# Kernel tuning notes

Measured on AMD Instinct MI355X. Metric: run time of the kernel, lower is better.

Reference implementation:

```python
import jax, jax.numpy as jnp
import numpy as np

L = 3          # atom_decoder_depth
HEADS = 8      # spatial attention heads
T_HEADS = 8    # temporal attention heads
WQ = 32        # atoms_per_window_queries
HK = 128       # atoms_per_window_keys
EPS = 1e-5


def _ln(x, g=None, b=None):
    mu = jnp.mean(x, -1, keepdims=True)
    v = jnp.mean((x - mu) ** 2, -1, keepdims=True)
    xn = (x - mu) * jax.lax.rsqrt(v + EPS)
    if g is not None:
        xn = xn * g + b
    return xn


def _adaln(a, s, w_sc, b_sc, w_sk):
    # adaptive LN: sigmoid-scaled normed activations + conditioned skip
    sn = _ln(s)
    return jax.nn.sigmoid(sn @ w_sc + b_sc) * _ln(a) + sn @ w_sk


def setup_inputs() -> dict:
    key = jax.random.key(0)
    ks = iter(jax.random.split(key, 64))
    B0, T, N, M, D, TS = 1, 8, 1024, 4096, 256, 768
    HID = 2 * D

    def rn(shape, s=1.0):
        return jax.random.normal(next(ks), shape, jnp.float32) * s

    NW = (M + WQ - 1) // WQ
    a = rn((B0 * T, N, 2 * TS))
    q = rn((B0 * T, M, D))
    c = rn((B0 * T, M, D))
    atom_dec_bias = rn((B0, NW, WQ, HK, L * HEADS), 0.1)
    tok_idx = jnp.sort(jax.random.randint(next(ks), (B0, M), 0, N), axis=-1)
    atom_to_token = jax.nn.one_hot(tok_idx, N, dtype=jnp.float32)
    atom_pad_mask = jnp.ones((B0, M), bool)
    timestamps = jnp.sort(jax.random.uniform(next(ks), (B0, T)) * 10.0, axis=-1)
    p = 0.02
    return dict(
        a=a, q=q, c=c, atom_dec_bias=atom_dec_bias,
        atom_to_token=atom_to_token, atom_pad_mask=atom_pad_mask,
        timestamps=timestamps,
        W_a2q=rn((2 * TS, D), p),
        ada1_sw=rn((L, D, D), p), ada1_sb=rn((L, D), p), ada1_kw=rn((L, D, D), p),
        attn_wq=rn((L, D, D), p), attn_bq=rn((L, D), p),
        attn_wk=rn((L, D, D), p), attn_wv=rn((L, D, D), p),
        attn_wg=rn((L, D, D), p), attn_wo=rn((L, D, D), p),
        og_w=rn((L, D, D), p), og_b=rn((L, D), p),
        ada2_sw=rn((L, D, D), p), ada2_sb=rn((L, D), p), ada2_kw=rn((L, D, D), p),
        tr_w1=rn((L, D, HID), p), tr_w2=rn((L, D, HID), p), tr_w3=rn((L, HID, D), p),
        tr_gw=rn((L, D, D), p), tr_gb=rn((L, D), p),
        t_ln_g=jnp.ones((L, D)), t_ln_b=jnp.zeros((L, D)),
        t_wq=rn((L, D, D), p), t_wk=rn((L, D, D), p), t_wv=rn((L, D, D), p),
        t_wg=rn((L, D, D), p), t_wo=rn((L, D, D), p),
        t_decay=rn((L, T_HEADS)),
        pos_g=jnp.ones((D,)), pos_b=jnp.zeros((D,)), pos_w=rn((D, 3), p),
        T=8,
    )


def _forward(a, q, c, atom_dec_bias, atom_to_token, atom_pad_mask, timestamps,
             W_a2q, ada1_sw, ada1_sb, ada1_kw, attn_wq, attn_bq, attn_wk,
             attn_wv, attn_wg, attn_wo, og_w, og_b, ada2_sw, ada2_sb, ada2_kw,
             tr_w1, tr_w2, tr_w3, tr_gw, tr_gb, t_ln_g, t_ln_b, t_wq, t_wk,
             t_wv, t_wg, t_wo, t_decay, pos_g, pos_b, pos_w, T):
    BT, N, _ = a.shape
    B0 = BT // T
    M0, D = q.shape[1], q.shape[2]
    NW = (M0 + WQ - 1) // WQ
    M = NW * WQ
    h, dh = HEADS, D // HEADS
    th, tdh = T_HEADS, D // T_HEADS

    # token -> atom gather via one-hot matmul (atom_to_token shared across T)
    a2q = jnp.einsum('bmn,btnd->btmd', atom_to_token,
                     (a @ W_a2q).reshape(B0, T, N, D)).reshape(BT, M0, D)
    q = q + a2q

    pad = M - M0
    qf = jnp.pad(q, ((0, 0), (0, pad), (0, 0)))
    cf = jnp.pad(c, ((0, 0), (0, pad), (0, 0)))
    mask = jnp.pad(atom_pad_mask, ((0, 0), (0, pad)))  # (B0, M)

    side = (HK - WQ) // 2
    # index map: query window w attends keys [w*WQ - side, w*WQ - side + HK)
    widx = jnp.arange(NW)[:, None] * WQ + jnp.arange(HK)[None, :]

    def window_keys(x):  # (B, M, D) -> (B, NW, HK, D)
        xp = jnp.pad(x, ((0, 0), (side, side), (0, 0)))
        return xp[:, widx]

    kmask = jnp.pad(mask, ((0, 0), (side, side)))[:, widx]  # (B0, NW, HK)
    neg = jnp.where(kmask[:, None, :, None, None, :], 0.0, -1e9)

    bias = atom_dec_bias.reshape(B0, NW, WQ, HK, L, HEADS)
    inv_s = 1.0 / np.sqrt(dh).astype(np.float32)
    inv_t = 1.0 / np.sqrt(tdh).astype(np.float32)
    dt = jnp.abs(timestamps[:, :, None] - timestamps[:, None, :])  # (B0,T,T)

    for i in range(L):
        # ---- spatial windowed attention with pair bias ----
        b = _adaln(qf, cf, ada1_sw[i], ada1_sb[i], ada1_kw[i])
        qh = (b @ attn_wq[i] + attn_bq[i]).reshape(BT, NW, WQ, h, dh)
        kin = window_keys(b)                                   # (BT,NW,HK,D)
        kh = (kin @ attn_wk[i]).reshape(BT, NW, HK, h, dh)
        vh = (kin @ attn_wv[i]).reshape(BT, NW, HK, h, dh)
        logits = jnp.einsum('bnqhd,bnkhd->bnhqk', qh, kh) * inv_s
        logits = logits.reshape(B0, T, NW, h, WQ, HK)
        logits = logits + bias[:, :, :, :, i].transpose(0, 1, 4, 2, 3)[:, None] + neg
        p_attn = jax.nn.softmax(logits, axis=-1).reshape(BT, NW, h, WQ, HK)
        o = jnp.einsum('bnhqk,bnkhd->bnqhd', p_attn, vh)
        g = jax.nn.sigmoid(b @ attn_wg[i]).reshape(BT, NW, WQ, h, dh)
        o = (g * o).reshape(BT, M, D) @ attn_wo[i]
        qf = qf + jax.nn.sigmoid(cf @ og_w[i] + og_b[i]) * o
        # conditioned SwiGLU transition
        t = _adaln(qf, cf, ada2_sw[i], ada2_sb[i], ada2_kw[i])
        x = jax.nn.silu(t @ tr_w1[i]) * (t @ tr_w2[i])
        qf = qf + jax.nn.sigmoid(cf @ tr_gw[i] + tr_gb[i]) * (x @ tr_w3[i])
        # ---- temporal attention with per-head decay bias ----
        xt = qf.reshape(B0, T, M, D).transpose(0, 2, 1, 3)     # (B0,M,T,D)
        xn = _ln(xt, t_ln_g[i], t_ln_b[i])
        tq = (xn @ t_wq[i]).reshape(B0, M, T, th, tdh)
        tk = (xn @ t_wk[i]).reshape(B0, M, T, th, tdh)
        tv = (xn @ t_wv[i]).reshape(B0, M, T, th, tdh)
        tl = jnp.einsum('bmqhd,bmkhd->bmhqk', tq, tk) * inv_t
        decay = jax.nn.softplus(t_decay[i])                    # (th,)
        tl = tl - decay[None, None, :, None, None] * dt[:, None, None]
        tp = jax.nn.softmax(tl, axis=-1)
        to = jnp.einsum('bmhqk,bmkhd->bmqhd', tp, tv).reshape(B0, M, T, D)
        tg = jax.nn.sigmoid(xn @ t_wg[i])
        xt = xt + (tg * to) @ t_wo[i]
        qf = xt.transpose(0, 2, 1, 3).reshape(BT, M, D)

    q_out = qf[:, :M0]
    return _ln(q_out, pos_g, pos_b) @ pos_w  # (B*T, M0, 3)


def reference(a, q, c, atom_dec_bias, atom_to_token, atom_pad_mask, timestamps,
              W_a2q, ada1_sw, ada1_sb, ada1_kw, attn_wq, attn_bq, attn_wk,
              attn_wv, attn_wg, attn_wo, og_w, og_b, ada2_sw, ada2_sb, ada2_kw,
              tr_w1, tr_w2, tr_w3, tr_gw, tr_gb, t_ln_g, t_ln_b, t_wq, t_wk,
              t_wv, t_wg, t_wo, t_decay, pos_g, pos_b, pos_w, T):
    return _forward(a, q, c, atom_dec_bias, atom_to_token, atom_pad_mask,
                    timestamps, W_a2q, ada1_sw, ada1_sb, ada1_kw, attn_wq,
                    attn_bq, attn_wk, attn_wv, attn_wg, attn_wo, og_w, og_b,
                    ada2_sw, ada2_sb, ada2_kw, tr_w1, tr_w2, tr_w3, tr_gw,
                    tr_gb, t_ln_g, t_ln_b, t_wq, t_wk, t_wv, t_wg, t_wo,
                    t_decay, pos_g, pos_b, pos_w, T)
```

## Files before the change

### kernel.cpp

```cpp
#include <hip/hip_runtime.h>
#include <cstddef>
#include <cstdint>

#define DEVI __device__ __forceinline__

typedef __attribute__((ext_vector_type(8))) __bf16 bf16x8;
typedef __attribute__((ext_vector_type(8))) unsigned short us8;
typedef __attribute__((ext_vector_type(4))) unsigned short us4;
typedef __attribute__((ext_vector_type(4))) float f32x4;

constexpr int B0_ = 1, T_ = 8, N_ = 1024, M_ = 4096, D_ = 256;
constexpr int BT_ = 8, NW_ = 128, WQ_ = 32, HK_ = 128, SIDE_ = 48;
constexpr int R_ = BT_ * M_;
constexpr size_t Fq = 8388608;

DEVI unsigned short f2b(float f) {
  return __builtin_bit_cast(unsigned short, static_cast<__bf16>(f));
}
DEVI float b2f(unsigned short s) { return __uint_as_float(((unsigned)s) << 16); }
DEVI float sigm(float x) { return 1.0f / (1.0f + __expf(-x)); }
DEVI bf16x8 ld_bf8(const unsigned short* p) {
  return __builtin_bit_cast(bf16x8, *(const us8*)p);
}
DEVI bf16x8 pack_f8(float4 v0, float4 v1) {
  bf16x8 r;
  r[0] = (__bf16)v0.x; r[1] = (__bf16)v0.y; r[2] = (__bf16)v0.z; r[3] = (__bf16)v0.w;
  r[4] = (__bf16)v1.x; r[5] = (__bf16)v1.y; r[6] = (__bf16)v1.z; r[7] = (__bf16)v1.w;
  return r;
}
DEVI void mfma_bf16(f32x4& c, bf16x8 a, bf16x8 b) {
  c = __builtin_amdgcn_mfma_f32_16x16x32_bf16(a, b, c, 0, 0, 0);
}
DEVI void gload16(const void* g, void* l) {
  __builtin_amdgcn_global_load_lds((__attribute__((address_space(1))) void*)g,
                                   (__attribute__((address_space(3))) void*)l, 16, 0, 0);
}

struct ConvArgs {
  const float* src[64];
  int doff[64];
  int Kd[64];
  int Nd[64];
  int n;
};

__global__ __launch_bounds__(256) void conv_k(ConvArgs ca, unsigned short* __restrict__ wbf) {
  int e = blockIdx.x;
  int K = ca.Kd[e], N = ca.Nd[e];
  int nx = N >> 6, nk = K >> 6;
  int t = blockIdx.y;
  if (t >= nx * nk) return;
  int tx = t % nx, tk = t / nx;
  const float* s = ca.src[e];
  unsigned short* d = wbf + ca.doff[e];
  int n = tx * 64 + (threadIdx.x & 63);
  int k0 = tk * 64 + (threadIdx.x >> 6) * 16;
  for (int r = 0; r < 16; r++) {
    int k = k0 + r;
    d[(size_t)n * K + k] = f2b(s[(size_t)k * N + n]);
  }
}

__global__ __launch_bounds__(256) void cvt_k(const float* __restrict__ s,
                                             unsigned short* __restrict__ d, int n8) {
  int i = blockIdx.x * 256 + threadIdx.x;
  if (i >= n8) return;
  float4 v0 = *(const float4*)(s + (size_t)i * 8);
  float4 v1 = *(const float4*)(s + (size_t)i * 8 + 4);
  *(us8*)(d + (size_t)i * 8) = __builtin_bit_cast(us8, pack_f8(v0, v1));
}

__global__ __launch_bounds__(256) void bias_prep_k(
    const float* __restrict__ bq, const float* __restrict__ sb1,
    const float* __restrict__ sb2, const float* __restrict__ ogb,
    const float* __restrict__ trb, float* __restrict__ bias) {
  int t = threadIdx.x;
  for (int i = t; i < 1024 + 3 * 2560; i += 256) bias[i] = 0.f;
  __syncthreads();
  for (int i = 0; i < 3; i++) {
    float* B = bias + 1024 + i * 2560;
    B[t]        = bq[i * 256 + t];
    B[1024 + t] = sb1[i * 256 + t];
    B[1536 + t] = sb2[i * 256 + t];
    B[2048 + t] = ogb[i * 256 + t];
    B[2304 + t] = trb[i * 256 + t];
  }
}

__global__ __launch_bounds__(256) void biasb_k(const float* __restrict__ adb,
                                               unsigned short* __restrict__ biasb) {
  __shared__ float ld[3072];
  int rq = blockIdx.x;
  int t = threadIdx.x;
  const float* src = adb + (size_t)rq * 3072;
  for (int i = t; i < 3072; i += 256) ld[i] = src[i];
  __syncthreads();
  int k = t & 127;
  int pk = (k & 15) * 8 + (k >> 4);
  for (int lh = t >> 7; lh < 24; lh += 2)
    biasb[((size_t)lh * 4096 + rq) * 128 + pk] = f2b(ld[k * 24 + lh]);
}

__global__ __launch_bounds__(256) void tokidx_k(const float* __restrict__ a2t,
                                                int* __restrict__ idx) {
  int m = blockIdx.x * 4 + (threadIdx.x >> 6);
  int lane = threadIdx.x & 63;
  int best = -1;
  for (int j = 0; j < 16; j++) {
    int col = lane * 16 + j;
    if (a2t[(size_t)m * 1024 + col] > 0.5f) best = col;
  }
#pragma unroll
  for (int off = 1; off < 64; off <<= 1) best = max(best, __shfl_xor(best, off));
  if (lane == 0) idx[m] = best;
}

__global__ __launch_bounds__(256) void qfinitln_k(const float* __restrict__ q,
                                                  const unsigned short* __restrict__ tokf,
                                                  const int* __restrict__ idx,
                                                  float* __restrict__ qf,
                                                  unsigned short* __restrict__ lnout) {
  int wid = threadIdx.x >> 6, lane = threadIdx.x & 63;
  size_t row = (size_t)blockIdx.x * 4 + wid;
  int m = (int)(row & 4095);
  int bt = (int)(row >> 12);
  float4 qv = *(const float4*)(q + row * 256 + lane * 4);
  us4 tv = *(const us4*)(tokf + ((size_t)bt * 1024 + idx[m]) * 256 + lane * 4);
  float x[4];
  x[0] = qv.x + b2f(tv[0]); x[1] = qv.y + b2f(tv[1]);
  x[2] = qv.z + b2f(tv[2]); x[3] = qv.w + b2f(tv[3]);
  *(float4*)(qf + row * 256 + lane * 4) = make_float4(x[0], x[1], x[2], x[3]);
  float s = x[0] + x[1] + x[2] + x[3];
  float sq = x[0] * x[0] + x[1] * x[1] + x[2] * x[2] + x[3] * x[3];
#pragma unroll
  for (int o = 1; o < 64; o <<= 1) {
    s += __shfl_xor(s, o);
    sq += __shfl_xor(sq, o);
  }
  float mu = s * 0.00390625f;
  float rs = rsqrtf(sq * 0.00390625f - mu * mu + 1e-5f);
  us4 r;
#pragma unroll
  for (int j = 0; j < 4; j++) r[j] = f2b((x[j] - mu) * rs);
  *(us4*)(lnout + row * 256 + lane * 4) = r;
}

__global__ __launch_bounds__(256) void ln_k(const float* __restrict__ src,
                                            unsigned short* __restrict__ dst) {
  size_t row = (size_t)blockIdx.x * 4 + (threadIdx.x >> 6);
  int lane = threadIdx.x & 63;
  float4 v = ((const float4*)(src + row * 256))[lane];
  float s = v.x + v.y + v.z + v.w;
#pragma unroll
  for (int o = 1; o < 64; o <<= 1) s += __shfl_xor(s, o);
  float mu = s * 0.00390625f;
  float dx = v.x - mu, dy = v.y - mu, dz = v.z - mu, dw = v.w - mu;
  float qv = dx * dx + dy * dy + dz * dz + dw * dw;
#pragma unroll
  for (int o = 1; o < 64; o <<= 1) qv += __shfl_xor(qv, o);
  float rs = rsqrtf(qv * 0.00390625f + 1e-5f);
  us4 r;
  r[0] = f2b(dx * rs); r[1] = f2b(dy * rs); r[2] = f2b(dz * rs); r[3] = f2b(dw * rs);
  *(us4*)(dst + row * 256 + lane * 4) = r;
}

template <int K, int EP, int PAIR>
__global__ __launch_bounds__(256) void gemm4_k(
    const unsigned short* __restrict__ A, const unsigned short* __restrict__ Wt,
    const float* __restrict__ bias, unsigned short* __restrict__ out,
    const unsigned short* __restrict__ lnq, unsigned short* __restrict__ vtb,
    int NOUT) {
  constexpr int NT = K / 64;
  __shared__ __align__(16) unsigned short S[2][16384];
  const int tid = threadIdx.x;
  const int lane = tid & 63, w = tid >> 6;
  const int lg = lane >> 4, lr = lane & 15;
  const int wr = w >> 1, wc = w & 1;
  const size_t m_base = (size_t)blockIdx.x * 128;
  const size_t n_base = (size_t)blockIdx.y * 64;
  const int srow = w * 8 + (lane >> 3);
  const int scol = ((lane & 7) ^ (lane >> 3)) * 8;
  const unsigned short* gA = A + (m_base + srow) * K + scol;
  const unsigned short* gB = Wt + (n_base + srow) * K + scol;
  const unsigned short* gB2 = Wt + (n_base + PAIR + srow) * K + scol;
  f32x4 acc[4][2] = {};
  f32x4 acc2[4][2] = {};
  const int swz = lr & 7;

  auto stage = [&](int buf, int t) {
    unsigned short* Sb = S[buf];
    const int kk = t * 64;
#pragma unroll
    for (int j = 0; j < 4; j++)
      gload16(gA + (size_t)(j * 32) * K + kk, Sb + w * 512 + j * 2048);
#pragma unroll
    for (int j = 0; j < 2; j++)
      gload16(gB + (size_t)(j * 32) * K + kk, Sb + 8192 + w * 512 + j * 2048);
#pragma unroll
    for (int j = 0; j < 2; j++)
      gload16(gB2 + (size_t)(j * 32) * K + kk, Sb + 12288 + w * 512 + j * 2048);
  };
  auto compute = [&](int buf) {
    const unsigned short* Sb = S[buf];
#pragma unroll
    for (int ks = 0; ks < 2; ks++) {
      const int co = ((ks * 4 + lg) ^ swz) << 3;
      bf16x8 af[4], b1[2], b2[2];
#pragma unroll
      for (int i = 0; i < 4; i++)
        af[i] = ld_bf8(Sb + (wr * 64 + i * 16 + lr) * 64 + co);
#pragma unroll
      for (int i = 0; i < 2; i++) {
        b1[i] = ld_bf8(Sb + 8192 + (wc * 32 + i * 16 + lr) * 64 + co);
        b2[i] = ld_bf8(Sb + 12288 + (wc * 32 + i * 16 + lr) * 64 + co);
      }
#pragma unroll
      for (int mi = 0; mi < 4; mi++)
#pragma unroll
        for (int ni = 0; ni < 2; ni++) {
          mfma_bf16(acc[mi][ni], af[mi], b1[ni]);
          mfma_bf16(acc2[mi][ni], af[mi], b2[ni]);
        }
    }
  };

  stage(0, 0);
  __syncthreads();
  int cur = 0;
  for (int t = 0; t < NT - 1; t++) {
    stage(cur ^ 1, t + 1);
    compute(cur);
    __syncthreads();
    cur ^= 1;
  }
  compute(cur);
  __syncthreads();

  unsigned short* St = S[0];
  auto emit_half = [&](int cbase, bool second) {
#pragma unroll
    for (int mi = 0; mi < 4; mi++)
#pragma unroll
      for (int ni = 0; ni < 2; ni++)
#pragma unroll
        for (int r = 0; r < 4; r++) {
          int rowl = wr * 64 + mi * 16 + lg * 4 + r;
          int cl = wc * 32 + ni * 16 + lr;
          float v = (second ? acc2[mi][ni][r] : acc[mi][ni][r]) + bias[cbase + cl];
          St[rowl * 64 + (((cl >> 3) ^ (rowl & 7)) << 3) + (cl & 7)] = f2b(v);
        }
    __syncthreads();
#pragma unroll
    for (int p = 0; p < 4; p++) {
      int rowl = p * 32 + (tid >> 3);
      int chunk = tid & 7;
      us8 v = *(const us8*)(St + rowl * 64 + ((chunk ^ (rowl & 7)) << 3));
      *(us8*)(out + (m_base + rowl) * NOUT + cbase + chunk * 8) = v;
    }
    __syncthreads();
  };

  if constexpr (EP == 1) {
    emit_half((int)n_base, false);
    emit_half((int)n_base + PAIR, true);
  } else if constexpr (EP == 6) {
    emit_half((int)n_base, false);
    if ((int)n_base < 256) {
      const int bt = (int)(m_base >> 12);
      const int m0 = (int)(m_base & 4095);
#pragma unroll
      for (int mi = 0; mi < 4; mi++)
#pragma unroll
        for (int ni = 0; ni < 2; ni++) {
          int cl = wc * 32 + ni * 16 + lr;
          int rowb = wr * 64 + mi * 16 + lg * 4;
          us4 val;
#pragma unroll
          for (int r = 0; r < 4; r++)
            val[r] = f2b(acc2[mi][ni][r] + bias[(int)n_base + cl + 512]);
          *(us4*)(St + cl * 128 + (((rowb >> 3) ^ (cl & 7)) << 3) + (rowb & 7)) = val;
        }
      __syncthreads();
#pragma unroll
      for (int p = 0; p < 4; p++) {
        int cl = tid >> 2;
        int rc = (tid & 3) + p * 4;
        us8 v = *(const us8*)(St + cl * 128 + ((rc ^ (cl & 7)) << 3));
        *(us8*)(vtb + ((size_t)bt * 256 + n_base + cl) * 4096 + m0 + rc * 8) = v;
      }
    } else {
      emit_half((int)n_base + 512, true);
    }
  } else {
#pragma unroll
    for (int mi = 0; mi < 4; mi++)
#pragma unroll
      for (int ni = 0; ni < 2; ni++)
#pragma unroll
        for (int r = 0; r < 4; r++) {
          int rowl = wr * 64 + mi * 16 + lg * 4 + r;
          int cl = wc * 32 + ni * 16 + lr;
          size_t grow = m_base + rowl;
          int gcol = (int)n_base + cl;
          float v = acc[mi][ni][r] + bias[gcol];
          float v2 = acc2[mi][ni][r] + bias[gcol + PAIR];
          unsigned short res;
          if constexpr (EP == 4) {
            res = f2b(sigm(v) * b2f(lnq[grow * 256 + gcol]) + v2);
          } else {
            res = f2b(v * sigm(v) * v2);
          }
          St[rowl * 64 + (((cl >> 3) ^ (rowl & 7)) << 3) + (cl & 7)] = res;
        }
    __syncthreads();
#pragma unroll
    for (int p = 0; p < 4; p++) {
      int rowl = p * 32 + (tid >> 3);
      int chunk = tid & 7;
      us8 v = *(const us8*)(St + rowl * 64 + ((chunk ^ (rowl & 7)) << 3));
      *(us8*)(out + (m_base + rowl) * NOUT + n_base + chunk * 8) = v;
    }
  }
}

template <int K, bool GATED>
__global__ __launch_bounds__(512) void gemmln_k(
    const unsigned short* __restrict__ A, const unsigned short* __restrict__ Wt,
    float* __restrict__ qf, const unsigned short* __restrict__ gate, int goff,
    unsigned short* __restrict__ lnout, const float* __restrict__ lng,
    const float* __restrict__ lnb) {
  constexpr int NT = K / 64;
  __shared__ __align__(16) unsigned short S[2][20480];
  const int tid = threadIdx.x;
  const int lane = tid & 63, w = tid >> 6;
  const int lg = lane >> 4, lr = lane & 15;
  const size_t m_base = (size_t)blockIdx.x * 64;
  const int srow = lane >> 3;
  const int scol = ((lane & 7) ^ srow) * 8;
  const unsigned short* gA = A + (m_base + w * 8 + srow) * K + scol;
  const unsigned short* gB = Wt + (w * 32 + srow) * K + scol;
  f32x4 acc[4][2] = {};
  const int swz = lr & 7;

  auto stage = [&](int buf, int t) {
    unsigned short* Sb = S[buf];
    const int kk = t * 64;
    gload16(gA + kk, Sb + w * 512);
#pragma unroll
    for (int j = 0; j < 4; j++)
      gload16(gB + (size_t)(j * 8) * K + kk, Sb + 4096 + w * 2048 + j * 512);
  };
  auto compute = [&](int buf) {
    const unsigned short* Sb = S[buf];
#pragma unroll
    for (int ks = 0; ks < 2; ks++) {
      const int co = ((ks * 4 + lg) ^ swz) << 3;
      bf16x8 af[4], bf1[2];
#pragma unroll
      for (int i = 0; i < 4; i++) af[i] = ld_bf8(Sb + (i * 16 + lr) * 64 + co);
#pragma unroll
      for (int i = 0; i < 2; i++)
        bf1[i] = ld_bf8(Sb + 4096 + (w * 32 + i * 16 + lr) * 64 + co);
#pragma unroll
      for (int mi = 0; mi < 4; mi++)
#pragma unroll
        for (int ni = 0; ni < 2; ni++) mfma_bf16(acc[mi][ni], af[mi], bf1[ni]);
    }
  };

  stage(0, 0);
  __syncthreads();
  int cur = 0;
  for (int t = 0; t < NT - 1; t++) {
    stage(cur ^ 1, t + 1);
    compute(cur);
    __syncthreads();
    cur ^= 1;
  }
  compute(cur);
  __syncthreads();

  unsigned short* St = S[0];
#pragma unroll
  for (int mi = 0; mi < 4; mi++)
#pragma unroll
    for (int ni = 0; ni < 2; ni++)
#pragma unroll
      for (int r = 0; r < 4; r++) {
        int rowl = mi * 16 + lg * 4 + r;
        int col = w * 32 + ni * 16 + lr;
        size_t grow = m_base + rowl;
        float v = acc[mi][ni][r];
        if constexpr (GATED) v *= sigm(b2f(gate[grow * 512 + goff + col]));
        float nq = qf[grow * 256 + col] + v;
        qf[grow * 256 + col] = nq;
        St[rowl * 256 + (((col >> 3) ^ (rowl & 7)) << 3) + (col & 7)] = f2b(nq);
      }
  __syncthreads();
  float gv[4], bv[4];
  if (lng) {
#pragma unroll
    for (int j = 0; j < 4; j++) {
      gv[j] = lng[lane * 4 + j];
      bv[j] = lnb[lane * 4 + j];
    }
  }
  const int rchunk = lane >> 1;
  const int rsub = (lane & 1) << 2;
  for (int rr = 0; rr < 8; rr++) {
    int rowl = w * 8 + rr;
    us4 vv = *(const us4*)(St + rowl * 256 + ((rchunk ^ (rowl & 7)) << 3) + rsub);
    float x[4];
#pragma unroll
    for (int j = 0; j < 4; j++) x[j] = b2f(vv[j]);
    float s = x[0] + x[1] + x[2] + x[3];
    float sq = x[0] * x[0] + x[1] * x[1] + x[2] * x[2] + x[3] * x[3];
#pragma unroll
    for (int o = 1; o < 64; o <<= 1) {
      s += __shfl_xor(s, o);
      sq += __shfl_xor(sq, o);
    }
    float mu = s * 0.00390625f;
    float rs = rsqrtf(sq * 0.00390625f - mu * mu + 1e-5f);
    us4 r;
#pragma unroll
    for (int j = 0; j < 4; j++) {
      float y = (x[j] - mu) * rs;
      if (lng) y = y * gv[j] + bv[j];
      r[j] = f2b(y);
    }
    *(us4*)(lnout + (m_base + rowl) * 256 + lane * 4) = r;
  }
}

__global__ __launch_bounds__(256) void attn_k(const unsigned short* __restrict__ big1,
                                              const unsigned short* __restrict__ vtbuf,
                                              const unsigned short* __restrict__ biasb,
                                              unsigned short* __restrict__ o, int layer) {
  __shared__ __align__(16) unsigned short pl_s[4][32 * 128];
  __shared__ __align__(16) unsigned short vt_s[4][32 * 128];
  const int bid = blockIdx.x;
  const int nid = (bid & 7) * 256 + (bid >> 3);
  const int w = nid & 127, bt = (nid >> 7) & 7, hg = nid >> 10;
  const int tid = threadIdx.x, wid = tid >> 6, lane = tid & 63;
  const int lg = lane >> 4, lr = lane & 15;
  const int h = hg * 4 + wid;
  unsigned short* pl = pl_s[wid];
  unsigned short* vt = vt_s[wid];
  const size_t base = (size_t)bt * M_;
  const float inv_s = 0.17677669529663687f;

  {
    const int d = lane >> 1, half = lane & 1;
    const unsigned short* src = vtbuf + ((size_t)bt * 256 + h * 32 + d) * 4096;
    const int k0 = w * 32 - SIDE_ + half * 64;
    unsigned short* dst = vt + d * 128;
#pragma unroll
    for (int c = 0; c < 8; c++) {
      int ak = k0 + c * 8;
      ak = ak < 0 ? 0 : (ak > M_ - 8 ? M_ - 8 : ak);
      us8 v = *(const us8*)(src + ak);
      const int chunk = half * 8 + c;
      *(us8*)(dst + ((chunk ^ (d & 7)) << 3)) = v;
    }
  }
  bf16x8 aq[2];
#pragma unroll
  for (int mi = 0; mi < 2; mi++)
    aq[mi] = ld_bf8(big1 + (base + w * 32 + mi * 16 + lr) * 1024 + h * 32 + lg * 8);
  f32x4 lac[2][8] = {};
#pragma unroll
  for (int ni = 0; ni < 8; ni++) {
    int kidx = ni * 16 + lr;
    int ak = w * 32 - SIDE_ + kidx;
    int akc = ak < 0 ? 0 : (ak > M_ - 1 ? M_ - 1 : ak);
    bf16x8 bk = ld_bf8(big1 + (base + akc) * 1024 + 256 + h * 32 + lg * 8);
    mfma_bf16(lac[0][ni], aq[0], bk);
    mfma_bf16(lac[1][ni], aq[1], bk);
  }
  const unsigned short* bb0 =
      biasb + (((size_t)(layer * 8 + h)) * 4096 + w * 32) * 128 + lr * 8;
#pragma unroll
  for (int mi = 0; mi < 2; mi++)
#pragma unroll
    for (int r = 0; r < 4; r++) {
      int qrow = mi * 16 + lg * 4 + r;
      us8 bb = *(const us8*)(bb0 + (size_t)qrow * 128);
      float lv[8];
      float mx = -3e38f;
#pragma unroll
      for (int ni = 0; ni < 8; ni++) {
        int ak = w * 32 - SIDE_ + ni * 16 + lr;
        float x = lac[mi][ni][r] * inv_s + b2f(bb[ni]) +
                  ((unsigned)ak < (unsigned)M_ ? 0.f : -1e9f);
        lv[ni] = x;
        mx = fmaxf(mx, x);
      }
#pragma unroll
      for (int off = 1; off < 16; off <<= 1) mx = fmaxf(mx, __shfl_xor(mx, off));
      float sum = 0.f;
#pragma unroll
      for (int ni = 0; ni < 8; ni++) {
        float e = __expf(lv[ni] - mx);
        lv[ni] = e;
        sum += e;
      }
#pragma unroll
      for (int off = 1; off < 16; off <<= 1) sum += __shfl_xor(sum, off);
      float inv = 1.f / sum;
      int sw = (qrow & 7) << 3;
#pragma unroll
      for (int ni = 0; ni < 8; ni++)
        pl[qrow * 128 + ((ni * 16 + lr) ^ sw)] = f2b(lv[ni] * inv);
    }
  f32x4 oc[2][2] = {};
#pragma unroll
  for (int ks = 0; ks < 4; ks++) {
    int kbase = ks * 32 + lg * 8;
    int kswz = kbase ^ ((lr & 7) << 3);
    bf16x8 ap0 = ld_bf8(pl + lr * 128 + kswz);
    bf16x8 ap1 = ld_bf8(pl + (16 + lr) * 128 + kswz);
    bf16x8 bv0 = ld_bf8(vt + lr * 128 + kswz);
    bf16x8 bv1 = ld_bf8(vt + (16 + lr) * 128 + kswz);
    mfma_bf16(oc[0][0], ap0, bv0);
    mfma_bf16(oc[0][1], ap0, bv1);
    mfma_bf16(oc[1][0], ap1, bv0);
    mfma_bf16(oc[1][1], ap1, bv1);
  }
#pragma unroll
  for (int mi = 0; mi < 2; mi++)
#pragma unroll
    for (int nd = 0; nd < 2; nd++)
#pragma unroll
      for (int r = 0; r < 4; r++) {
        int qrow = mi * 16 + lg * 4 + r;
        int d = nd * 16 + lr;
        size_t rowi = base + w * 32 + qrow;
        float gv = sigm(b2f(big1[rowi * 1024 + 768 + h * 32 + d]));
        o[rowi * 256 + h * 32 + d] = f2b(oc[mi][nd][r] * gv);
      }
}

__global__ __launch_bounds__(256) void tattn_k(const unsigned short* __restrict__ big1,
                                               const float* __restrict__ ts,
                                               const float* __restrict__ tdec,
                                               unsigned short* __restrict__ o, int layer) {
  __shared__ __align__(16) unsigned short lds[4][8 * 768];
  int wid = threadIdx.x >> 6, lane = threadIdx.x & 63;
  int m = blockIdx.x * 4 + wid;
  unsigned short* Lp = lds[wid];
  for (int it = 0; it < 12; it++) {
    int u = it * 64 + lane;
    int t = u / 96, pos = (u % 96) * 8;
    *(uint4*)(Lp + t * 768 + pos) =
        *(const uint4*)(big1 + ((size_t)(t * M_ + m)) * 1024 + pos);
  }
  __syncthreads();
  int th = lane >> 3, qt = lane & 7;
  float decay = log1pf(__expf(tdec[layer * 8 + th]));
  float tsq = ts[qt];
  const float inv_t = 0.17677669529663687f;
  float tqv[32];
#pragma unroll
  for (int d = 0; d < 32; d++) tqv[d] = b2f(Lp[qt * 768 + th * 32 + d]);
  float lv[8];
  float mx = -3e38f;
#pragma unroll
  for (int kt = 0; kt < 8; kt++) {
    float dot = 0.f;
#pragma unroll
    for (int d = 0; d < 32; d++) dot += tqv[d] * b2f(Lp[kt * 768 + 256 + th * 32 + d]);
    float x = dot * inv_t - decay * fabsf(tsq - ts[kt]);
    lv[kt] = x;
    mx = fmaxf(mx, x);
  }
  float s = 0.f;
#pragma unroll
  for (int kt = 0; kt < 8; kt++) {
    float e = __expf(lv[kt] - mx);
    lv[kt] = e;
    s += e;
  }
  float inv = 1.f / s;
  float tov[32];
#pragma unroll
  for (int d = 0; d < 32; d++) tov[d] = 0.f;
#pragma unroll
  for (int kt = 0; kt < 8; kt++) {
    float p = lv[kt] * inv;
#pragma unroll
    for (int d = 0; d < 32; d++) tov[d] += p * b2f(Lp[kt * 768 + 512 + th * 32 + d]);
  }
  size_t orow = (size_t)qt * M_ + m;
#pragma unroll
  for (int d = 0; d < 32; d++) {
    float tg = sigm(b2f(big1[orow * 1024 + 768 + th * 32 + d]));
    o[orow * 256 + th * 32 + d] = f2b(tov[d] * tg);
  }
}

__global__ __launch_bounds__(256) void final_k(const float* __restrict__ qf,
                                               const float* __restrict__ pg,
                                               const float* __restrict__ pb,
                                               const float* __restrict__ pw,
                                               float* __restrict__ out) {
  size_t row = (size_t)blockIdx.x * 4 + (threadIdx.x >> 6);
  int lane = threadIdx.x & 63;
  float4 v = ((const float4*)(qf + row * 256))[lane];
  float s = v.x + v.y + v.z + v.w;
#pragma unroll
  for (int o = 1; o < 64; o <<= 1) s += __shfl_xor(s, o);
  float mu = s * 0.00390625f;
  float dx = v.x - mu, dy = v.y - mu, dz = v.z - mu, dw = v.w - mu;
  float qv = dx * dx + dy * dy + dz * dz + dw * dw;
#pragma unroll
  for (int o = 1; o < 64; o <<= 1) qv += __shfl_xor(qv, o);
  float rs = rsqrtf(qv * 0.00390625f + 1e-5f);
  int d = lane * 4;
  float xn[4];
  xn[0] = dx * rs * pg[d] + pb[d];
  xn[1] = dy * rs * pg[d + 1] + pb[d + 1];
  xn[2] = dz * rs * pg[d + 2] + pb[d + 2];
  xn[3] = dw * rs * pg[d + 3] + pb[d + 3];
  float p0 = 0.f, p1 = 0.f, p2 = 0.f;
#pragma unroll
  for (int dd = 0; dd < 4; dd++) {
    const float* wr = pw + (size_t)(d + dd) * 3;
    p0 += xn[dd] * wr[0];
    p1 += xn[dd] * wr[1];
    p2 += xn[dd] * wr[2];
  }
#pragma unroll
  for (int o = 1; o < 64; o <<= 1) {
    p0 += __shfl_xor(p0, o);
    p1 += __shfl_xor(p1, o);
    p2 += __shfl_xor(p2, o);
  }
  if (lane == 0) {
    out[row * 3 + 0] = p0;
    out[row * 3 + 1] = p1;
    out[row * 3 + 2] = p2;
  }
}

extern "C" void kernel_launch(void* const* d_in, const int* in_sizes, int n_in,
                              void* d_out, int out_size, void* d_ws, size_t ws_size,
                              hipStream_t stream) {
  const float* a       = (const float*)d_in[0];
  const float* q_in    = (const float*)d_in[1];
  const float* c_in    = (const float*)d_in[2];
  const float* adb     = (const float*)d_in[3];
  const float* a2t     = (const float*)d_in[4];
  const float* ts      = (const float*)d_in[6];
  const float* W_a2q   = (const float*)d_in[7];
  const float* ada1_sw = (const float*)d_in[8];
  const float* ada1_sb = (const float*)d_in[9];
  const float* ada1_kw = (const float*)d_in[10];
  const float* attn_wq = (const float*)d_in[11];
  const float* attn_bq = (const float*)d_in[12];
  const float* attn_wk = (const float*)d_in[13];
  const float* attn_wv = (const float*)d_in[14];
  const float* attn_wg = (const float*)d_in[15];
  const float* attn_wo = (const float*)d_in[16];
  const float* og_w    = (const float*)d_in[17];
  const float* og_b    = (const float*)d_in[18];
  const float* ada2_sw = (const float*)d_in[19];
  const float* ada2_sb = (const float*)d_in[20];
  const float* ada2_kw = (const float*)d_in[21];
  const float* tr_w1   = (const float*)d_in[22];
  const float* tr_w2   = (const float*)d_in[23];
  const float* tr_w3   = (const float*)d_in[24];
  const float* tr_gw   = (const float*)d_in[25];
  const float* tr_gb   = (const float*)d_in[26];
  const float* t_ln_g  = (const float*)d_in[27];
  const float* t_ln_b  = (const float*)d_in[28];
  const float* t_wq    = (const float*)d_in[29];
  const float* t_wk    = (const float*)d_in[30];
  const float* t_wv    = (const float*)d_in[31];
  const float* t_wg    = (const float*)d_in[32];
  const float* t_wo    = (const float*)d_in[33];
  const float* t_dec   = (const float*)d_in[34];
  const float* pos_g   = (const float*)d_in[35];
  const float* pos_b   = (const float*)d_in[36];
  const float* pos_w   = (const float*)d_in[37];

  char* base = (char*)d_ws;
  size_t off = 0;
  auto alloc = [&](size_t bytes) {
    void* p = base + off;
    off += (bytes + 255) & ~(size_t)255;
    return p;
  };
  float* qf            = (float*)alloc(Fq * 4);
  unsigned short* lncb = (unsigned short*)alloc(Fq * 2);
  unsigned short* lnqb = (unsigned short*)alloc(Fq * 2);
  unsigned short* obuf = (unsigned short*)alloc(Fq * 2);
  unsigned short* big1 = (unsigned short*)alloc(Fq * 8);
  unsigned short* bbuf = (unsigned short*)alloc(Fq * 2);
  unsigned short* cbf  = (unsigned short*)alloc(Fq * 2);
  unsigned short* vtbuf= (unsigned short*)alloc(Fq * 2);
  unsigned short* biasb= (unsigned short*)alloc((size_t)24 * 4096 * 128 * 2);
  unsigned short* wbf  = (unsigned short*)alloc((size_t)4718592 * 2);
  float* biasr         = (float*)alloc(8704 * 4);
  int* tokidx          = (int*)alloc(4096 * 4);

  unsigned short* xbuf  = big1;
  unsigned short* ggate = big1 + (size_t)R_ * 512;
  unsigned short* abf   = big1;
  unsigned short* tokf  = big1 + 2 * Fq;

  ConvArgs ca;
  int ne = 0;
  auto add = [&](const float* s, size_t doff, int K, int N) {
    ca.src[ne] = s; ca.doff[ne] = (int)doff; ca.Kd[ne] = K; ca.Nd[ne] = N; ne++;
  };
  constexpr size_t LW = 1441792;
  for (int i = 0; i < 3; i++) {
    size_t LB = (size_t)i * LW;
    add(ada1_sw + i * 65536, LB + 0, 256, 256);
    add(ada1_kw + i * 65536, LB + 65536, 256, 256);
    add(attn_wq + i * 65536, LB + 131072, 256, 256);
    add(attn_wk + i * 65536, LB + 196608, 256, 256);
    add(attn_wv + i * 65536, LB + 262144, 256, 256);
    add(attn_wg + i * 65536, LB + 327680, 256, 256);
    add(attn_wo + i * 65536, LB + 393216, 256, 256);
    add(og_w + i * 65536, LB + 458752, 256, 256);
    add(tr_gw + i * 65536, LB + 524288, 256, 256);
    add(ada2_sw + i * 65536, LB + 589824, 256, 256);
    add(ada2_kw + i * 65536, LB + 655360, 256, 256);
    add(tr_w1 + i * 131072, LB + 720896, 256, 512);
    add(tr_w2 + i * 131072, LB + 851968, 256, 512);
    add(tr_w3 + i * 131072, LB + 983040, 512, 256);
    add(t_wq + i * 65536, LB + 1114112, 256, 256);
    add(t_wk + i * 65536, LB + 1179648, 256, 256);
    add(t_wv + i * 65536, LB + 1245184, 256, 256);
    add(t_wg + i * 65536, LB + 1310720, 256, 256);
    add(t_wo + i * 65536, LB + 1376256, 256, 256);
  }
  add(W_a2q, 3 * LW, 1536, 256);
  ca.n = ne;

  conv_k<<<dim3(ne, 96), 256, 0, stream>>>(ca, wbf);
  bias_prep_k<<<1, 256, 0, stream>>>(attn_bq, ada1_sb, ada2_sb, og_b, tr_gb, biasr);
  tokidx_k<<<1024, 256, 0, stream>>>(a2t, tokidx);
  biasb_k<<<4096, 256, 0, stream>>>(adb, biasb);
  cvt_k<<<6144, 256, 0, stream>>>(a, abf, 1572864);
  cvt_k<<<4096, 256, 0, stream>>>(c_in, cbf, 1048576);
  gemm4_k<1536, 1, 128><<<dim3(64, 2), 256, 0, stream>>>(
      abf, wbf + 3 * LW, biasr, tokf, nullptr, nullptr, 256);
  qfinitln_k<<<8192, 256, 0, stream>>>(q_in, tokf, tokidx, qf, lnqb);
  ln_k<<<8192, 256, 0, stream>>>(c_in, lncb);

  for (int i = 0; i < 3; i++) {
    size_t LB = (size_t)i * LW;
    const float* b_attn = biasr + 1024 + (size_t)i * 2560;
    const float* b_ada1 = b_attn + 1024;
    const float* b_ada2 = b_attn + 1536;
    const float* b_ogtr = b_attn + 2048;

    gemm4_k<256, 4, 256><<<dim3(256, 4), 256, 0, stream>>>(
        lncb, wbf + LB, b_ada1, bbuf, lnqb, nullptr, 256);
    gemm4_k<256, 6, 512><<<dim3(256, 8), 256, 0, stream>>>(
        bbuf, wbf + LB + 131072, b_attn, big1, nullptr, vtbuf, 1024);
    attn_k<<<2048, 256, 0, stream>>>(big1, vtbuf, biasb, obuf, i);
    gemm4_k<256, 1, 256><<<dim3(256, 4), 256, 0, stream>>>(
        cbf, wbf + LB + 458752, b_ogtr, ggate, nullptr, nullptr, 512);
    gemmln_k<256, true><<<512, 512, 0, stream>>>(
        obuf, wbf + LB + 393216, qf, ggate, 0, lnqb, nullptr, nullptr);
    gemm4_k<256, 4, 256><<<dim3(256, 4), 256, 0, stream>>>(
        lncb, wbf + LB + 589824, b_ada2, bbuf, lnqb, nullptr, 256);
    gemm4_k<256, 5, 512><<<dim3(256, 8), 256, 0, stream>>>(
        bbuf, wbf + LB + 720896, biasr, xbuf, nullptr, nullptr, 512);
    gemmln_k<512, true><<<512, 512, 0, stream>>>(
        xbuf, wbf + LB + 983040, qf, ggate, 256, lnqb,
        t_ln_g + (size_t)i * 256, t_ln_b + (size_t)i * 256);
    gemm4_k<256, 1, 512><<<dim3(256, 8), 256, 0, stream>>>(
        lnqb, wbf + LB + 1114112, biasr, big1, nullptr, nullptr, 1024);
    tattn_k<<<1024, 256, 0, stream>>>(big1, ts, t_dec, obuf, i);
    gemmln_k<256, false><<<512, 512, 0, stream>>>(
        obuf, wbf + LB + 1376256, qf, nullptr, 0, lnqb, nullptr, nullptr);
  }
  final_k<<<8192, 256, 0, stream>>>(qf, pos_g, pos_b, pos_w, (float*)d_out);
}
```

Before: 1.144 ms.

## Fold attention scale and mask into preprocessing, drop V LDS staging, add setprio

The 1/sqrt(d) softmax scale is folded into the bf16 query weights and query bias during weight conversion, and the window-boundary mask is baked into the precomputed bf16 pair bias. This removes the per-element scale and mask arithmetic from the attention softmax. The attention kernel no longer stages V into shared memory; it reads V directly from global memory inside the PV loop and defers softmax normalization to the output write. s_setprio hints are also added around MFMA blocks in the GEMM and attention kernels. The trade-off is small rounding differences from scaling before bf16 conversion, a -1e9 mask stored in bf16, and possibly slower uncoalesced global V loads.

```diff
diff --git a/kernel.cpp b/kernel.cpp
--- a/kernel.cpp
+++ b/kernel.cpp
@@ -41,6 +41,7 @@
   int doff[64];
   int Kd[64];
   int Nd[64];
+  float scale[64];
   int n;
 };
 
@@ -52,12 +53,13 @@
   if (t >= nx * nk) return;
   int tx = t % nx, tk = t / nx;
   const float* s = ca.src[e];
+  float sc = ca.scale[e];
   unsigned short* d = wbf + ca.doff[e];
   int n = tx * 64 + (threadIdx.x & 63);
   int k0 = tk * 64 + (threadIdx.x >> 6) * 16;
   for (int r = 0; r < 16; r++) {
     int k = k0 + r;
-    d[(size_t)n * K + k] = f2b(s[(size_t)k * N + n]);
+    d[(size_t)n * K + k] = f2b(s[(size_t)k * N + n] * sc);
   }
 }
 
@@ -75,11 +77,12 @@
     const float* __restrict__ sb2, const float* __restrict__ ogb,
     const float* __restrict__ trb, float* __restrict__ bias) {
   int t = threadIdx.x;
+  const float inv_s = 0.17677669529663687f;
   for (int i = t; i < 1024 + 3 * 2560; i += 256) bias[i] = 0.f;
   __syncthreads();
   for (int i = 0; i < 3; i++) {
     float* B = bias + 1024 + i * 2560;
-    B[t]        = bq[i * 256 + t];
+    B[t]        = bq[i * 256 + t] * inv_s;
     B[1024 + t] = sb1[i * 256 + t];
     B[1536 + t] = sb2[i * 256 + t];
     B[2048 + t] = ogb[i * 256 + t];
@@ -97,8 +100,10 @@
   __syncthreads();
   int k = t & 127;
   int pk = (k & 15) * 8 + (k >> 4);
+  int ak = (rq >> 5) * 32 - SIDE_ + k;
+  float maskv = ((unsigned)ak < (unsigned)M_) ? 0.f : -1e9f;
   for (int lh = t >> 7; lh < 24; lh += 2)
-    biasb[((size_t)lh * 4096 + rq) * 128 + pk] = f2b(ld[k * 24 + lh]);
+    biasb[((size_t)lh * 4096 + rq) * 128 + pk] = f2b(ld[k * 24 + lh] + maskv);
 }
 
 __global__ __launch_bounds__(256) void tokidx_k(const float* __restrict__ a2t,
@@ -214,6 +219,7 @@
         b1[i] = ld_bf8(Sb + 8192 + (wc * 32 + i * 16 + lr) * 64 + co);
         b2[i] = ld_bf8(Sb + 12288 + (wc * 32 + i * 16 + lr) * 64 + co);
       }
+      __builtin_amdgcn_s_setprio(1);
 #pragma unroll
       for (int mi = 0; mi < 4; mi++)
 #pragma unroll
@@ -221,6 +227,7 @@
           mfma_bf16(acc[mi][ni], af[mi], b1[ni]);
           mfma_bf16(acc2[mi][ni], af[mi], b2[ni]);
         }
+      __builtin_amdgcn_s_setprio(0);
     }
   };
 
@@ -361,10 +368,12 @@
 #pragma unroll
       for (int i = 0; i < 2; i++)
         bf1[i] = ld_bf8(Sb + 4096 + (w * 32 + i * 16 + lr) * 64 + co);
+      __builtin_amdgcn_s_setprio(1);
 #pragma unroll
       for (int mi = 0; mi < 4; mi++)
 #pragma unroll
         for (int ni = 0; ni < 2; ni++) mfma_bf16(acc[mi][ni], af[mi], bf1[ni]);
+      __builtin_amdgcn_s_setprio(0);
     }
   };
 
@@ -438,7 +447,6 @@
                                               const unsigned short* __restrict__ biasb,
                                               unsigned short* __restrict__ o, int layer) {
   __shared__ __align__(16) unsigned short pl_s[4][32 * 128];
-  __shared__ __align__(16) unsigned short vt_s[4][32 * 128];
   const int bid = blockIdx.x;
   const int nid = (bid & 7) * 256 + (bid >> 3);
   const int w = nid & 127, bt = (nid >> 7) & 7, hg = nid >> 10;
@@ -446,24 +454,8 @@
   const int lg = lane >> 4, lr = lane & 15;
   const int h = hg * 4 + wid;
   unsigned short* pl = pl_s[wid];
-  unsigned short* vt = vt_s[wid];
   const size_t base = (size_t)bt * M_;
-  const float inv_s = 0.17677669529663687f;
-
-  {
-    const int d = lane >> 1, half = lane & 1;
-    const unsigned short* src = vtbuf + ((size_t)bt * 256 + h * 32 + d) * 4096;
-    const int k0 = w * 32 - SIDE_ + half * 64;
-    unsigned short* dst = vt + d * 128;
-#pragma unroll
-    for (int c = 0; c < 8; c++) {
-      int ak = k0 + c * 8;
-      ak = ak < 0 ? 0 : (ak > M_ - 8 ? M_ - 8 : ak);
-      us8 v = *(const us8*)(src + ak);
-      const int chunk = half * 8 + c;
-      *(us8*)(dst + ((chunk ^ (d & 7)) << 3)) = v;
-    }
-  }
+
   bf16x8 aq[2];
 #pragma unroll
   for (int mi = 0; mi < 2; mi++)
@@ -475,11 +467,14 @@
     int ak = w * 32 - SIDE_ + kidx;
     int akc = ak < 0 ? 0 : (ak > M_ - 1 ? M_ - 1 : ak);
     bf16x8 bk = ld_bf8(big1 + (base + akc) * 1024 + 256 + h * 32 + lg * 8);
+    __builtin_amdgcn_s_setprio(1);
     mfma_bf16(lac[0][ni], aq[0], bk);
     mfma_bf16(lac[1][ni], aq[1], bk);
+    __builtin_amdgcn_s_setprio(0);
   }
   const unsigned short* bb0 =
       biasb + (((size_t)(layer * 8 + h)) * 4096 + w * 32) * 128 + lr * 8;
+  float invs[2][4];
 #pragma unroll
   for (int mi = 0; mi < 2; mi++)
 #pragma unroll
@@ -490,9 +485,7 @@
       float mx = -3e38f;
 #pragma unroll
       for (int ni = 0; ni < 8; ni++) {
-        int ak = w * 32 - SIDE_ + ni * 16 + lr;
-        float x = lac[mi][ni][r] * inv_s + b2f(bb[ni]) +
-                  ((unsigned)ak < (unsigned)M_ ? 0.f : -1e9f);
+        float x = lac[mi][ni][r] + b2f(bb[ni]);
         lv[ni] = x;
         mx = fmaxf(mx, x);
       }
@@ -507,25 +500,30 @@
       }
 #pragma unroll
       for (int off = 1; off < 16; off <<= 1) sum += __shfl_xor(sum, off);
-      float inv = 1.f / sum;
+      invs[mi][r] = 1.f / sum;
       int sw = (qrow & 7) << 3;
 #pragma unroll
       for (int ni = 0; ni < 8; ni++)
-        pl[qrow * 128 + ((ni * 16 + lr) ^ sw)] = f2b(lv[ni] * inv);
-    }
+        pl[qrow * 128 + ((ni * 16 + lr) ^ sw)] = f2b(lv[ni]);
+    }
+  const unsigned short* vrow0 = vtbuf + ((size_t)bt * 256 + h * 32 + lr) * 4096;
+  const unsigned short* vrow1 = vrow0 + (size_t)16 * 4096;
   f32x4 oc[2][2] = {};
 #pragma unroll
   for (int ks = 0; ks < 4; ks++) {
-    int kbase = ks * 32 + lg * 8;
-    int kswz = kbase ^ ((lr & 7) << 3);
+    int kcol = w * 32 - SIDE_ + ks * 32 + lg * 8;
+    kcol = kcol < 0 ? 0 : (kcol > M_ - 8 ? M_ - 8 : kcol);
+    bf16x8 bv0 = ld_bf8(vrow0 + kcol);
+    bf16x8 bv1 = ld_bf8(vrow1 + kcol);
+    int kswz = (ks * 32 + lg * 8) ^ ((lr & 7) << 3);
     bf16x8 ap0 = ld_bf8(pl + lr * 128 + kswz);
     bf16x8 ap1 = ld_bf8(pl + (16 + lr) * 128 + kswz);
-    bf16x8 bv0 = ld_bf8(vt + lr * 128 + kswz);
-    bf16x8 bv1 = ld_bf8(vt + (16 + lr) * 128 + kswz);
+    __builtin_amdgcn_s_setprio(1);
     mfma_bf16(oc[0][0], ap0, bv0);
     mfma_bf16(oc[0][1], ap0, bv1);
     mfma_bf16(oc[1][0], ap1, bv0);
     mfma_bf16(oc[1][1], ap1, bv1);
+    __builtin_amdgcn_s_setprio(0);
   }
 #pragma unroll
   for (int mi = 0; mi < 2; mi++)
@@ -537,7 +535,7 @@
         int d = nd * 16 + lr;
         size_t rowi = base + w * 32 + qrow;
         float gv = sigm(b2f(big1[rowi * 1024 + 768 + h * 32 + d]));
-        o[rowi * 256 + h * 32 + d] = f2b(oc[mi][nd][r] * gv);
+        o[rowi * 256 + h * 32 + d] = f2b(oc[mi][nd][r] * invs[mi][r] * gv);
       }
 }
 
@@ -711,33 +709,35 @@
 
   ConvArgs ca;
   int ne = 0;
-  auto add = [&](const float* s, size_t doff, int K, int N) {
-    ca.src[ne] = s; ca.doff[ne] = (int)doff; ca.Kd[ne] = K; ca.Nd[ne] = N; ne++;
+  auto add = [&](const float* s, size_t doff, int K, int N, float sc) {
+    ca.src[ne] = s; ca.doff[ne] = (int)doff; ca.Kd[ne] = K; ca.Nd[ne] = N;
+    ca.scale[ne] = sc; ne++;
   };
+  const float inv_s = 0.17677669529663687f;
   constexpr size_t LW = 1441792;
   for (int i = 0; i < 3; i++) {
     size_t LB = (size_t)i * LW;
-    add(ada1_sw + i * 65536, LB + 0, 256, 256);
-    add(ada1_kw + i * 65536, LB + 65536, 256, 256);
-    add(attn_wq + i * 65536, LB + 131072, 256, 256);
-    add(attn_wk + i * 65536, LB + 196608, 256, 256);
-    add(attn_wv + i * 65536, LB + 262144, 256, 256);
-    add(attn_wg + i * 65536, LB + 327680, 256, 256);
-    add(attn_wo + i * 65536, LB + 393216, 256, 256);
-    add(og_w + i * 65536, LB + 458752, 256, 256);
-    add(tr_gw + i * 65536, LB + 524288, 256, 256);
-    add(ada2_sw + i * 65536, LB + 589824, 256, 256);
-    add(ada2_kw + i * 65536, LB + 655360, 256, 256);
-    add(tr_w1 + i * 131072, LB + 720896, 256, 512);
-    add(tr_w2 + i * 131072, LB + 851968, 256, 512);
-    add(tr_w3 + i * 131072, LB + 983040, 512, 256);
-    add(t_wq + i * 65536, LB + 1114112, 256, 256);
-    add(t_wk + i * 65536, LB + 1179648, 256, 256);
-    add(t_wv + i * 65536, LB + 1245184, 256, 256);
-    add(t_wg + i * 65536, LB + 1310720, 256, 256);
-    add(t_wo + i * 65536, LB + 1376256, 256, 256);
-  }
-  add(W_a2q, 3 * LW, 1536, 256);
+    add(ada1_sw + i * 65536, LB + 0, 256, 256, 1.f);
+    add(ada1_kw + i * 65536, LB + 65536, 256, 256, 1.f);
+    add(attn_wq + i * 65536, LB + 131072, 256, 256, inv_s);
+    add(attn_wk + i * 65536, LB + 196608, 256, 256, 1.f);
+    add(attn_wv + i * 65536, LB + 262144, 256, 256, 1.f);
+    add(attn_wg + i * 65536, LB + 327680, 256, 256, 1.f);
+    add(attn_wo + i * 65536, LB + 393216, 256, 256, 1.f);
+    add(og_w + i * 65536, LB + 458752, 256, 256, 1.f);
+    add(tr_gw + i * 65536, LB + 524288, 256, 256, 1.f);
+    add(ada2_sw + i * 65536, LB + 589824, 256, 256, 1.f);
+    add(ada2_kw + i * 65536, LB + 655360, 256, 256, 1.f);
+    add(tr_w1 + i * 131072, LB + 720896, 256, 512, 1.f);
+    add(tr_w2 + i * 131072, LB + 851968, 256, 512, 1.f);
+    add(tr_w3 + i * 131072, LB + 983040, 512, 256, 1.f);
+    add(t_wq + i * 65536, LB + 1114112, 256, 256, 1.f);
+    add(t_wk + i * 65536, LB + 1179648, 256, 256, 1.f);
+    add(t_wv + i * 65536, LB + 1245184, 256, 256, 1.f);
+    add(t_wg + i * 65536, LB + 1310720, 256, 256, 1.f);
+    add(t_wo + i * 65536, LB + 1376256, 256, 256, 1.f);
+  }
+  add(W_a2q, 3 * LW, 1536, 256, 1.f);
   ca.n = ne;
 
   conv_k<<<dim3(ne, 96), 256, 0, stream>>>(ca, wbf);
```

Result: no change. 1.123 ms (-1.8%).
